# Optimization experiments

Measured on AMD Instinct MI355X. Metric: run time of the kernel, lower is better.

Reference implementation:

```python
import jax, jax.numpy as jnp
import numpy as np

N, K, D = 65536, 256, 512
ALPHA = 1.0

def setup_inputs() -> dict:
    key = jax.random.key(0)
    k1, k2 = jax.random.split(key)
    inputs = jax.random.normal(k1, (N, D), dtype=jnp.float32)
    clusters = jax.random.normal(k2, (K, D), dtype=jnp.float32)
    return {"inputs": inputs, "clusters": clusters}

def reference(inputs, clusters):
    # sum((x[:,None]-c[None])**2, -1), avoids the O(N*K*D) broadcast intermediate)
    x2 = jnp.sum(inputs * inputs, axis=1, keepdims=True)          # [N,1]
    c2 = jnp.sum(clusters * clusters, axis=1)                      # [K]
    xc = jnp.einsum('nd,kd->nk', inputs, clusters)                 # [N,K]
    dist = jnp.maximum(x2 + c2[None, :] - 2.0 * xc, 0.0)           # clamp fp error
    q = 1.0 / (1.0 + dist / ALPHA)
    q = q ** ((ALPHA + 1.0) / 2.0)
    q = q / jnp.sum(q, axis=1, keepdims=True)
    return q
```

## Files before the change

kernel.cpp:

```cpp
#include <hip/hip_runtime.h>
#include <hip/hip_bf16.h>

typedef short bf16x8 __attribute__((ext_vector_type(8)));
typedef float f32x4 __attribute__((ext_vector_type(4)));

constexpr int Nn = 65536;
constexpr int Kk = 256;
constexpr int Dd = 512;
constexpr int BM = 64;
constexpr int BK = 64;

static __device__ __forceinline__ unsigned short f2bf(float f) {
  __hip_bfloat16 h = __float2bfloat16(f);
  return *reinterpret_cast<unsigned short*>(&h);
}

static __device__ __forceinline__ void rbar() {
  asm volatile("s_waitcnt lgkmcnt(0)" ::: "memory");
  __builtin_amdgcn_s_barrier();
  asm volatile("" ::: "memory");
}

__global__ __launch_bounds__(64)
void prep_clusters_kernel(const float* __restrict__ C,
                          unsigned short* __restrict__ CB,
                          float* __restrict__ c2) {
  const int k = blockIdx.x;
  const int t = threadIdx.x;
  const float* row = C + (size_t)k * Dd;
  float4 a = *reinterpret_cast<const float4*>(row + t * 8);
  float4 b = *reinterpret_cast<const float4*>(row + t * 8 + 4);
  float s = a.x * a.x + a.y * a.y + a.z * a.z + a.w * a.w
          + b.x * b.x + b.y * b.y + b.z * b.z + b.w * b.w;
  uint4 p;
  p.x = ((unsigned)f2bf(a.y) << 16) | f2bf(a.x);
  p.y = ((unsigned)f2bf(a.w) << 16) | f2bf(a.z);
  p.z = ((unsigned)f2bf(b.y) << 16) | f2bf(b.x);
  p.w = ((unsigned)f2bf(b.w) << 16) | f2bf(b.z);
  *reinterpret_cast<uint4*>(CB + (size_t)k * Dd + t * 8) = p;
  #pragma unroll
  for (int m = 1; m < 64; m <<= 1) s += __shfl_xor(s, m, 64);
  if (t == 0) c2[k] = s;
}

__global__ __launch_bounds__(256, 2)
void cluster_q_kernel(const float* __restrict__ X,
                      const unsigned short* __restrict__ CB,
                      const float* __restrict__ c2g,
                      float* __restrict__ out) {
  __shared__ __align__(16) char Al[2][BM * BK * 2];
  __shared__ float x2s[BM];
  __shared__ __align__(16) float rowp[BM][4];

  const int tid  = threadIdx.x;
  const int lane = tid & 63;
  const int wave = tid >> 6;
  const int hi   = lane >> 4;
  const int lo   = lane & 15;
  const int rbase = blockIdx.x * BM;
  const int arow  = tid >> 4;
  const int acolb = (tid & 15) * 8;

  f32x4 acc[4][4];
  #pragma unroll
  for (int m = 0; m < 4; ++m)
    #pragma unroll
    for (int n = 0; n < 4; ++n)
      #pragma unroll
      for (int r = 0; r < 4; ++r) acc[m][n][r] = 0.f;

  float x2p[4] = {0.f, 0.f, 0.f, 0.f};
  float4 v[4];
  bf16x8 bA[4][2], bB[4][2];

  auto loadG = [&](int ks) {
    #pragma unroll
    for (int it = 0; it < 4; ++it)
      v[it] = *reinterpret_cast<const float4*>(
          &X[(size_t)(rbase + it * 16 + arow) * Dd + ks * BK + (tid & 15) * 4]);
  };

  auto stage = [&](int buf) {
    #pragma unroll
    for (int it = 0; it < 4; ++it) {
      const int row = it * 16 + arow;
      float4 f = v[it];
      x2p[it] += f.x * f.x + f.y * f.y + f.z * f.z + f.w * f.w;
      uint2 p;
      p.x = ((unsigned)f2bf(f.y) << 16) | f2bf(f.x);
      p.y = ((unsigned)f2bf(f.w) << 16) | f2bf(f.z);
      const int addr = (row * 128 + acolb) ^ ((row & 7) << 4);
      *reinterpret_cast<uint2*>(&Al[buf][addr]) = p;
    }
  };

  auto loadB = [&](int ks, bf16x8 (&bf)[4][2]) {
    #pragma unroll
    for (int n = 0; n < 4; ++n)
      #pragma unroll
      for (int ku = 0; ku < 2; ++ku)
        bf[n][ku] = *reinterpret_cast<const bf16x8*>(
            &CB[(size_t)(wave * 64 + n * 16 + lo) * Dd + ks * BK + ku * 32 + hi * 8]);
  };

  auto compute = [&](int buf, bf16x8 (&bf)[4][2]) {
    #pragma unroll
    for (int ku = 0; ku < 2; ++ku) {
      bf16x8 af[4];
      #pragma unroll
      for (int m = 0; m < 4; ++m) {
        const int row = m * 16 + lo;
        const int addr = (row * 128 + ku * 64 + hi * 16) ^ ((row & 7) << 4);
        af[m] = *reinterpret_cast<const bf16x8*>(&Al[buf][addr]);
      }
      #pragma unroll
      for (int m = 0; m < 4; ++m)
        #pragma unroll
        for (int n = 0; n < 4; ++n)
          acc[m][n] = __builtin_amdgcn_mfma_f32_16x16x32_bf16(af[m], bf[n][ku], acc[m][n], 0, 0, 0);
    }
  };

  loadG(0);
  stage(0);
  loadG(1);
  loadB(0, bA);
  rbar();

  auto iter = [&](int ks, bf16x8 (&bcur)[4][2], bf16x8 (&bnxt)[4][2]) {
    if (ks < 7) stage((ks + 1) & 1);
    if (ks < 6) loadG(ks + 2);
    if (ks < 7) loadB(ks + 1, bnxt);
    compute(ks & 1, bcur);
    rbar();
  };

  #pragma unroll
  for (int p = 0; p < 4; ++p) {
    iter(2 * p, bA, bB);
    iter(2 * p + 1, bB, bA);
  }

  #pragma unroll
  for (int it = 0; it < 4; ++it) {
    float s = x2p[it];
    s += __shfl_xor(s, 1); s += __shfl_xor(s, 2);
    s += __shfl_xor(s, 4); s += __shfl_xor(s, 8);
    if ((tid & 15) == 0) x2s[it * 16 + arow] = s;
  }
  __syncthreads();

  float c2v[4];
  #pragma unroll
  for (int n = 0; n < 4; ++n) c2v[n] = c2g[wave * 64 + n * 16 + lo];

  float rs[4][4];
  #pragma unroll
  for (int m = 0; m < 4; ++m)
    #pragma unroll
    for (int r = 0; r < 4; ++r) rs[m][r] = 0.f;

  #pragma unroll
  for (int m = 0; m < 4; ++m) {
    #pragma unroll
    for (int n = 0; n < 4; ++n) {
      #pragma unroll
      for (int r = 0; r < 4; ++r) {
        const int row = m * 16 + hi * 4 + r;
        float dist = x2s[row] + c2v[n] - 2.f * acc[m][n][r];
        dist = fmaxf(dist, 0.f);
        float qv = __builtin_amdgcn_rcpf(1.f + dist);
        acc[m][n][r] = qv;
        rs[m][r] += qv;
      }
    }
  }

  #pragma unroll
  for (int m = 0; m < 4; ++m)
    #pragma unroll
    for (int r = 0; r < 4; ++r) {
      float s = rs[m][r];
      s += __shfl_xor(s, 1); s += __shfl_xor(s, 2);
      s += __shfl_xor(s, 4); s += __shfl_xor(s, 8);
      rs[m][r] = s;
    }

  if (lo == 0) {
    #pragma unroll
    for (int m = 0; m < 4; ++m)
      #pragma unroll
      for (int r = 0; r < 4; ++r)
        rowp[m * 16 + hi * 4 + r][wave] = rs[m][r];
  }
  __syncthreads();

  float rinv[4][4];
  #pragma unroll
  for (int m = 0; m < 4; ++m)
    #pragma unroll
    for (int r = 0; r < 4; ++r) {
      float4 t = *reinterpret_cast<float4*>(rowp[m * 16 + hi * 4 + r]);
      rinv[m][r] = __builtin_amdgcn_rcpf(t.x + t.y + t.z + t.w);
    }

  #pragma unroll
  for (int m = 0; m < 4; ++m)
    #pragma unroll
    for (int n = 0; n < 4; ++n)
      #pragma unroll
      for (int r = 0; r < 4; ++r) {
        const int row = m * 16 + hi * 4 + r;
        out[(size_t)(rbase + row) * Kk + wave * 64 + n * 16 + lo] = acc[m][n][r] * rinv[m][r];
      }
}

extern "C" void kernel_launch(void* const* d_in, const int* in_sizes, int n_in,
                              void* d_out, int out_size, void* d_ws, size_t ws_size,
                              hipStream_t stream) {
  const float* X = reinterpret_cast<const float*>(d_in[0]);
  const float* C = reinterpret_cast<const float*>(d_in[1]);
  unsigned short* CB = reinterpret_cast<unsigned short*>(d_ws);
  float* c2 = reinterpret_cast<float*>(reinterpret_cast<char*>(d_ws) + (size_t)Kk * Dd * 2);
  prep_clusters_kernel<<<Kk, 64, 0, stream>>>(C, CB, c2);
  cluster_q_kernel<<<Nn / BM, 256, 0, stream>>>(X, CB, c2, reinterpret_cast<float*>(d_out));
}
```

Before: 61.76 us.

## Halve row tile to 32, raise occupancy, restructure X and B prefetch pipeline

Cuts the block row tile from 64 to 32 rows, which halves the accumulator registers, and raises the launch-bounds occupancy hint from 2 to 3 blocks. The X prefetch becomes two-deep with double-buffered registers. The cluster B fragments now use a single register set loaded in the same iteration they are consumed, instead of being prefetched one step ahead. The aim is more resident waves to hide memory latency and twice as many blocks. In exchange each cluster tile is reloaded for every 32 rows instead of every 64, and the B load latency is no longer hidden behind the previous step's compute.

```diff
diff --git a/kernel.cpp b/kernel.cpp
--- a/kernel.cpp
+++ b/kernel.cpp
@@ -7,7 +7,7 @@
 constexpr int Nn = 65536;
 constexpr int Kk = 256;
 constexpr int Dd = 512;
-constexpr int BM = 64;
+constexpr int BM = 32;
 constexpr int BK = 64;
 
 static __device__ __forceinline__ unsigned short f2bf(float f) {
@@ -43,7 +43,7 @@
   if (t == 0) c2[k] = s;
 }
 
-__global__ __launch_bounds__(256, 2)
+__global__ __launch_bounds__(256, 3)
 void cluster_q_kernel(const float* __restrict__ X,
                       const unsigned short* __restrict__ CB,
                       const float* __restrict__ c2g,
@@ -61,88 +61,82 @@
   const int arow  = tid >> 4;
   const int acolb = (tid & 15) * 8;
 
-  f32x4 acc[4][4];
-  #pragma unroll
-  for (int m = 0; m < 4; ++m)
+  f32x4 acc[2][4];
+  #pragma unroll
+  for (int m = 0; m < 2; ++m)
     #pragma unroll
     for (int n = 0; n < 4; ++n)
       #pragma unroll
       for (int r = 0; r < 4; ++r) acc[m][n][r] = 0.f;
 
-  float x2p[4] = {0.f, 0.f, 0.f, 0.f};
-  float4 v[4];
-  bf16x8 bA[4][2], bB[4][2];
+  float x2p[2] = {0.f, 0.f};
+  float4 v[2][2];
+  bf16x8 bB[4][2];
 
   auto loadG = [&](int ks) {
     #pragma unroll
-    for (int it = 0; it < 4; ++it)
-      v[it] = *reinterpret_cast<const float4*>(
+    for (int it = 0; it < 2; ++it)
+      v[ks & 1][it] = *reinterpret_cast<const float4*>(
           &X[(size_t)(rbase + it * 16 + arow) * Dd + ks * BK + (tid & 15) * 4]);
   };
 
-  auto stage = [&](int buf) {
-    #pragma unroll
-    for (int it = 0; it < 4; ++it) {
+  auto stage = [&](int ks) {
+    #pragma unroll
+    for (int it = 0; it < 2; ++it) {
       const int row = it * 16 + arow;
-      float4 f = v[it];
+      float4 f = v[ks & 1][it];
       x2p[it] += f.x * f.x + f.y * f.y + f.z * f.z + f.w * f.w;
       uint2 p;
       p.x = ((unsigned)f2bf(f.y) << 16) | f2bf(f.x);
       p.y = ((unsigned)f2bf(f.w) << 16) | f2bf(f.z);
       const int addr = (row * 128 + acolb) ^ ((row & 7) << 4);
-      *reinterpret_cast<uint2*>(&Al[buf][addr]) = p;
-    }
-  };
-
-  auto loadB = [&](int ks, bf16x8 (&bf)[4][2]) {
+      *reinterpret_cast<uint2*>(&Al[ks & 1][addr]) = p;
+    }
+  };
+
+  auto loadB = [&](int ks) {
     #pragma unroll
     for (int n = 0; n < 4; ++n)
       #pragma unroll
       for (int ku = 0; ku < 2; ++ku)
-        bf[n][ku] = *reinterpret_cast<const bf16x8*>(
+        bB[n][ku] = *reinterpret_cast<const bf16x8*>(
             &CB[(size_t)(wave * 64 + n * 16 + lo) * Dd + ks * BK + ku * 32 + hi * 8]);
   };
 
-  auto compute = [&](int buf, bf16x8 (&bf)[4][2]) {
+  auto compute = [&](int ks) {
     #pragma unroll
     for (int ku = 0; ku < 2; ++ku) {
-      bf16x8 af[4];
-      #pragma unroll
-      for (int m = 0; m < 4; ++m) {
+      bf16x8 af[2];
+      #pragma unroll
+      for (int m = 0; m < 2; ++m) {
         const int row = m * 16 + lo;
         const int addr = (row * 128 + ku * 64 + hi * 16) ^ ((row & 7) << 4);
-        af[m] = *reinterpret_cast<const bf16x8*>(&Al[buf][addr]);
+        af[m] = *reinterpret_cast<const bf16x8*>(&Al[ks & 1][addr]);
       }
       #pragma unroll
-      for (int m = 0; m < 4; ++m)
+      for (int m = 0; m < 2; ++m)
         #pragma unroll
         for (int n = 0; n < 4; ++n)
-          acc[m][n] = __builtin_amdgcn_mfma_f32_16x16x32_bf16(af[m], bf[n][ku], acc[m][n], 0, 0, 0);
+          acc[m][n] = __builtin_amdgcn_mfma_f32_16x16x32_bf16(af[m], bB[n][ku], acc[m][n], 0, 0, 0);
     }
   };
 
   loadG(0);
+  loadG(1);
   stage(0);
-  loadG(1);
-  loadB(0, bA);
   rbar();
 
-  auto iter = [&](int ks, bf16x8 (&bcur)[4][2], bf16x8 (&bnxt)[4][2]) {
-    if (ks < 7) stage((ks + 1) & 1);
+  #pragma unroll
+  for (int ks = 0; ks < 8; ++ks) {
+    if (ks < 7) stage(ks + 1);
+    loadB(ks);
     if (ks < 6) loadG(ks + 2);
-    if (ks < 7) loadB(ks + 1, bnxt);
-    compute(ks & 1, bcur);
+    compute(ks);
     rbar();
-  };
-
-  #pragma unroll
-  for (int p = 0; p < 4; ++p) {
-    iter(2 * p, bA, bB);
-    iter(2 * p + 1, bB, bA);
-  }
-
-  #pragma unroll
-  for (int it = 0; it < 4; ++it) {
+  }
+
+  #pragma unroll
+  for (int it = 0; it < 2; ++it) {
     float s = x2p[it];
     s += __shfl_xor(s, 1); s += __shfl_xor(s, 2);
     s += __shfl_xor(s, 4); s += __shfl_xor(s, 8);
@@ -154,14 +148,14 @@
   #pragma unroll
   for (int n = 0; n < 4; ++n) c2v[n] = c2g[wave * 64 + n * 16 + lo];
 
-  float rs[4][4];
-  #pragma unroll
-  for (int m = 0; m < 4; ++m)
+  float rs[2][4];
+  #pragma unroll
+  for (int m = 0; m < 2; ++m)
     #pragma unroll
     for (int r = 0; r < 4; ++r) rs[m][r] = 0.f;
 
   #pragma unroll
-  for (int m = 0; m < 4; ++m) {
+  for (int m = 0; m < 2; ++m) {
     #pragma unroll
     for (int n = 0; n < 4; ++n) {
       #pragma unroll
@@ -177,7 +171,7 @@
   }
 
   #pragma unroll
-  for (int m = 0; m < 4; ++m)
+  for (int m = 0; m < 2; ++m)
     #pragma unroll
     for (int r = 0; r < 4; ++r) {
       float s = rs[m][r];
@@ -188,16 +182,16 @@
 
   if (lo == 0) {
     #pragma unroll
-    for (int m = 0; m < 4; ++m)
+    for (int m = 0; m < 2; ++m)
       #pragma unroll
       for (int r = 0; r < 4; ++r)
         rowp[m * 16 + hi * 4 + r][wave] = rs[m][r];
   }
   __syncthreads();
 
-  float rinv[4][4];
-  #pragma unroll
-  for (int m = 0; m < 4; ++m)
+  float rinv[2][4];
+  #pragma unroll
+  for (int m = 0; m < 2; ++m)
     #pragma unroll
     for (int r = 0; r < 4; ++r) {
       float4 t = *reinterpret_cast<float4*>(rowp[m * 16 + hi * 4 + r]);
@@ -205,7 +199,7 @@
     }
 
   #pragma unroll
-  for (int m = 0; m < 4; ++m)
+  for (int m = 0; m < 2; ++m)
     #pragma unroll
     for (int n = 0; n < 4; ++n)
       #pragma unroll
```

New measurement: 83.12 us. 1.35x slower.

## Deepen global prefetch of X to three stages with ordered issue

Applied to the files above, without the earlier changes.

The X tile register prefetch goes from two stages ahead to three, with a triple-buffered register array. Cluster B-fragment loads are now issued before staging, and compiler fences fix the issue order. The aim is to hide more global memory latency behind the MFMA work. The cost is higher register pressure: 16 more VGPRs of float4 data under launch bounds of 2 blocks per CU, which could cause spills.

```diff
diff --git a/kernel.cpp b/kernel.cpp
--- a/kernel.cpp
+++ b/kernel.cpp
@@ -15,10 +15,12 @@
   return *reinterpret_cast<unsigned short*>(&h);
 }
 
+static __device__ __forceinline__ void fence() { asm volatile("" ::: "memory"); }
+
 static __device__ __forceinline__ void rbar() {
   asm volatile("s_waitcnt lgkmcnt(0)" ::: "memory");
   __builtin_amdgcn_s_barrier();
-  asm volatile("" ::: "memory");
+  fence();
 }
 
 __global__ __launch_bounds__(64)
@@ -70,27 +72,27 @@
       for (int r = 0; r < 4; ++r) acc[m][n][r] = 0.f;
 
   float x2p[4] = {0.f, 0.f, 0.f, 0.f};
-  float4 v[4];
+  float4 v[3][4];
   bf16x8 bA[4][2], bB[4][2];
 
   auto loadG = [&](int ks) {
     #pragma unroll
     for (int it = 0; it < 4; ++it)
-      v[it] = *reinterpret_cast<const float4*>(
+      v[ks % 3][it] = *reinterpret_cast<const float4*>(
           &X[(size_t)(rbase + it * 16 + arow) * Dd + ks * BK + (tid & 15) * 4]);
   };
 
-  auto stage = [&](int buf) {
+  auto stage = [&](int ks) {
     #pragma unroll
     for (int it = 0; it < 4; ++it) {
       const int row = it * 16 + arow;
-      float4 f = v[it];
+      float4 f = v[ks % 3][it];
       x2p[it] += f.x * f.x + f.y * f.y + f.z * f.z + f.w * f.w;
       uint2 p;
       p.x = ((unsigned)f2bf(f.y) << 16) | f2bf(f.x);
       p.y = ((unsigned)f2bf(f.w) << 16) | f2bf(f.z);
       const int addr = (row * 128 + acolb) ^ ((row & 7) << 4);
-      *reinterpret_cast<uint2*>(&Al[buf][addr]) = p;
+      *reinterpret_cast<uint2*>(&Al[ks & 1][addr]) = p;
     }
   };
 
@@ -103,7 +105,7 @@
             &CB[(size_t)(wave * 64 + n * 16 + lo) * Dd + ks * BK + ku * 32 + hi * 8]);
   };
 
-  auto compute = [&](int buf, bf16x8 (&bf)[4][2]) {
+  auto compute = [&](int ks, bf16x8 (&bf)[4][2]) {
     #pragma unroll
     for (int ku = 0; ku < 2; ++ku) {
       bf16x8 af[4];
@@ -111,7 +113,7 @@
       for (int m = 0; m < 4; ++m) {
         const int row = m * 16 + lo;
         const int addr = (row * 128 + ku * 64 + hi * 16) ^ ((row & 7) << 4);
-        af[m] = *reinterpret_cast<const bf16x8*>(&Al[buf][addr]);
+        af[m] = *reinterpret_cast<const bf16x8*>(&Al[ks & 1][addr]);
       }
       #pragma unroll
       for (int m = 0; m < 4; ++m)
@@ -121,17 +123,18 @@
     }
   };
 
-  loadG(0);
+  loadG(0); fence();
+  loadG(1); fence();
+  loadG(2); fence();
+  loadB(0, bA); fence();
   stage(0);
-  loadG(1);
-  loadB(0, bA);
   rbar();
 
   auto iter = [&](int ks, bf16x8 (&bcur)[4][2], bf16x8 (&bnxt)[4][2]) {
-    if (ks < 7) stage((ks + 1) & 1);
-    if (ks < 6) loadG(ks + 2);
-    if (ks < 7) loadB(ks + 1, bnxt);
-    compute(ks & 1, bcur);
+    if (ks < 7) { loadB(ks + 1, bnxt); fence(); }
+    if (ks < 7) { stage(ks + 1); fence(); }
+    if (ks < 5) { loadG(ks + 3); fence(); }
+    compute(ks, bcur);
     rbar();
   };
 
```

New measurement: 69.41 us. 12.4% more time.
